# Kernel optimization log

Measured on AMD Instinct MI355X. Metric: run time of the kernel, lower is better.

The kernel has to match this reference:

```python
import jax, jax.numpy as jnp
import numpy as np

N_NODES = 50000
N_EDGES = 800000
D = 64
NEG_SLOPE = 0.01  # torch F.leaky_relu default


def _gin_layer(h, src, dst, eps, W, b, activate):
    # max-aggregate neighbor features: for each dst node, max over incoming src feats
    msg = h[src]  # [E, D] gather
    agg = jax.ops.segment_max(msg, dst, num_segments=N_NODES)  # [N, D]
    # DGL fills nodes with no in-edges with 0 for max reduce
    agg = jnp.where(jnp.isfinite(agg), agg, jnp.zeros((), h.dtype))
    out = ((1.0 + eps) * h + agg) @ W + b
    if activate:
        out = jnp.where(out >= 0, out, NEG_SLOPE * out)
    return out


def setup_inputs() -> dict:
    key = jax.random.key(0)
    ks = jax.random.split(key, 6)
    scale = 1.0 / np.sqrt(D)
    return {
        "n_feat": jax.random.normal(ks[0], (N_NODES, D), dtype=jnp.float32),
        "W0": jax.random.normal(ks[1], (D, D), dtype=jnp.float32) * scale,
        "b0": jnp.zeros((D,), jnp.float32),
        "W1": jax.random.normal(ks[2], (D, D), dtype=jnp.float32) * scale,
        "b1": jnp.zeros((D,), jnp.float32),
        "W2": jax.random.normal(ks[3], (D, D), dtype=jnp.float32) * scale,
        "b2": jnp.zeros((D,), jnp.float32),
        "eps": jnp.zeros((3,), jnp.float32),
        "src": jax.random.randint(ks[4], (N_EDGES,), 0, N_NODES, dtype=jnp.int32),
        "dst": jax.random.randint(ks[5], (N_EDGES,), 0, N_NODES, dtype=jnp.int32),
    }


def reference(n_feat, W0, b0, W1, b1, W2, b2, eps, src, dst):
    h = _gin_layer(n_feat, src, dst, eps[0], W0, b0, activate=True)
    h = _gin_layer(h, src, dst, eps[1], W1, b1, activate=True)
    h = _gin_layer(h, src, dst, eps[2], W2, b2, activate=False)  # last_activate=False
    return h
```

## Files before the change

kernel.cpp:

```cpp
#include <hip/hip_runtime.h>

#define N_NODES 50000
#define N_EDGES 800000
#define D 64
#define CAP 64
#define XLD 72

typedef short short8 __attribute__((ext_vector_type(8)));
typedef float floatx4 __attribute__((ext_vector_type(4)));
typedef unsigned short ushort_t;

__device__ __forceinline__ ushort_t f32_to_bf16(float f) {
    unsigned int u = __float_as_uint(f);
    u += 0x7FFFu + ((u >> 16) & 1u);
    return (ushort_t)(u >> 16);
}
__device__ __forceinline__ float bf16lo(unsigned int u) { return __uint_as_float(u << 16); }
__device__ __forceinline__ float bf16hi(unsigned int u) { return __uint_as_float(u & 0xFFFF0000u); }

__global__ void __launch_bounds__(256) cvtw_kernel(const float* __restrict__ in,
                                                   ushort_t* __restrict__ hb0,
                                                   const float* __restrict__ W0,
                                                   const float* __restrict__ W1,
                                                   const float* __restrict__ W2,
                                                   ushort_t* __restrict__ wt_all) {
    int t = blockIdx.x * 256 + threadIdx.x;
    float4 v = ((const float4*)in)[t];
    uint2 o;
    o.x = ((unsigned)f32_to_bf16(v.y) << 16) | f32_to_bf16(v.x);
    o.y = ((unsigned)f32_to_bf16(v.w) << 16) | f32_to_bf16(v.z);
    ((uint2*)hb0)[t] = o;
    if (blockIdx.x < 3) {
        const float* Ws[3] = {W0, W1, W2};
        const float* W = Ws[blockIdx.x];
        ushort_t* ow = wt_all + blockIdx.x * 4096;
        for (int idx = threadIdx.x; idx < 4096; idx += 256) {
            int k = idx >> 6, n = idx & 63;
            ow[n * 64 + k] = f32_to_bf16(W[idx]);
        }
    }
}

__global__ void __launch_bounds__(256) fill_kernel(const int* __restrict__ src,
                                                   const int* __restrict__ dst,
                                                   int* __restrict__ cnt,
                                                   ushort_t* __restrict__ bucket) {
    int e = blockIdx.x * 256 + threadIdx.x;
    int t = dst[e];
    int slot = atomicAdd(&cnt[t], 1);
    if (slot < CAP) bucket[t * CAP + slot] = (ushort_t)src[e];
}

__global__ void __launch_bounds__(256) layer_kernel(
        const ushort_t* __restrict__ hin,
        const int* __restrict__ cnt,
        const ushort_t* __restrict__ bucket,
        const ushort_t* __restrict__ wt,
        const float* __restrict__ bias,
        const float* __restrict__ eps_arr,
        int layer, int activate, int last,
        ushort_t* __restrict__ out_bf,
        float* __restrict__ out_f32) {
    __shared__ ushort_t bk[16 * CAP];
    __shared__ ushort_t xs[16 * XLD];

    const int tid = threadIdx.x;
    const int lane = tid & 63;
    const int wv = tid >> 6;
    const int grp = lane >> 4;
    const int fo = (lane & 15) * 4;
    const float ev = 1.0f + eps_arr[layer];

    const int r0 = blockIdx.x * 16 + wv * 4;

#pragma unroll
    for (int j = 0; j < 4; ++j)
        bk[(wv * 4 + j) * CAP + lane] = bucket[(r0 + j) * CAP + lane];

    const int rr = r0 + grp;
    int cg = min(cnt[rr], CAP);
    int c0 = __builtin_amdgcn_readlane(cg, 0);
    int c1 = __builtin_amdgcn_readlane(cg, 16);
    int c2 = __builtin_amdgcn_readlane(cg, 32);
    int c3 = __builtin_amdgcn_readlane(cg, 48);
    int cmax = max(max(c0, c1), max(c2, c3));

    const uint2 sv = *(const uint2*)&hin[rr * 64 + fo];

    float m0 = -INFINITY, m1 = -INFINITY, m2 = -INFINITY, m3 = -INFINITY;
    const ushort_t* bkrow = &bk[(wv * 4 + grp) * CAP];
    for (int i = 0; i < cmax; ++i) {
        if (i < cg) {
            int s = bkrow[i];
            const uint2 u = *(const uint2*)&hin[s * 64 + fo];
            m0 = fmaxf(m0, bf16lo(u.x)); m1 = fmaxf(m1, bf16hi(u.x));
            m2 = fmaxf(m2, bf16lo(u.y)); m3 = fmaxf(m3, bf16hi(u.y));
        }
    }
    float a0 = (cg > 0) ? m0 : 0.f, a1 = (cg > 0) ? m1 : 0.f;
    float a2 = (cg > 0) ? m2 : 0.f, a3 = (cg > 0) ? m3 : 0.f;
    float x0 = fmaf(ev, bf16lo(sv.x), a0), x1 = fmaf(ev, bf16hi(sv.x), a1);
    float x2 = fmaf(ev, bf16lo(sv.y), a2), x3 = fmaf(ev, bf16hi(sv.y), a3);
    uint2 w;
    w.x = ((unsigned)f32_to_bf16(x1) << 16) | f32_to_bf16(x0);
    w.y = ((unsigned)f32_to_bf16(x3) << 16) | f32_to_bf16(x2);
    *(uint2*)&xs[(wv * 4 + grp) * XLD + fo] = w;
    __syncthreads();

    const int l15 = lane & 15, hi = lane >> 4;
    const int kc = hi * 8;
    short8 fa0 = *(const short8*)&xs[l15 * XLD + kc];
    short8 fa1 = *(const short8*)&xs[l15 * XLD + 32 + kc];
    const int ncol = wv * 16 + l15;
    short8 fb0 = *(const short8*)&wt[ncol * 64 + kc];
    short8 fb1 = *(const short8*)&wt[ncol * 64 + 32 + kc];
    floatx4 acc = {0.f, 0.f, 0.f, 0.f};
    acc = __builtin_amdgcn_mfma_f32_16x16x32_bf16(fa0, fb0, acc, 0, 0, 0);
    acc = __builtin_amdgcn_mfma_f32_16x16x32_bf16(fa1, fb1, acc, 0, 0, 0);

    const float bv = bias[ncol];
#pragma unroll
    for (int i = 0; i < 4; ++i) {
        int grow = blockIdx.x * 16 + hi * 4 + i;
        float v = acc[i] + bv;
        if (activate) v = (v >= 0.f) ? v : 0.01f * v;
        if (last) out_f32[(size_t)grow * 64 + ncol] = v;
        else out_bf[(size_t)grow * 64 + ncol] = f32_to_bf16(v);
    }
}

extern "C" void kernel_launch(void* const* d_in, const int* in_sizes, int n_in,
                              void* d_out, int out_size, void* d_ws, size_t ws_size,
                              hipStream_t stream) {
    const float* n_feat = (const float*)d_in[0];
    const float* W0 = (const float*)d_in[1];
    const float* b0 = (const float*)d_in[2];
    const float* W1 = (const float*)d_in[3];
    const float* b1 = (const float*)d_in[4];
    const float* W2 = (const float*)d_in[5];
    const float* b2 = (const float*)d_in[6];
    const float* eps = (const float*)d_in[7];
    const int* src = (const int*)d_in[8];
    const int* dst = (const int*)d_in[9];
    float* out = (float*)d_out;

    const size_t BKT_OFF = 200192;
    const size_t HB0_OFF = BKT_OFF + (size_t)N_NODES * CAP * 2;
    const size_t HB1_OFF = HB0_OFF + (size_t)N_NODES * 64 * 2;
    const size_t WT_OFF  = HB1_OFF + (size_t)N_NODES * 64 * 2;

    int* cnt = (int*)d_ws;
    ushort_t* bucket = (ushort_t*)((char*)d_ws + BKT_OFF);
    ushort_t* hb0 = (ushort_t*)((char*)d_ws + HB0_OFF);
    ushort_t* hb1 = (ushort_t*)((char*)d_ws + HB1_OFF);
    ushort_t* wt_all = (ushort_t*)((char*)d_ws + WT_OFF);

    hipMemsetAsync(cnt, 0, (size_t)N_NODES * 4, stream);
    cvtw_kernel<<<3125, 256, 0, stream>>>(n_feat, hb0, W0, W1, W2, wt_all);
    fill_kernel<<<N_EDGES / 256, 256, 0, stream>>>(src, dst, cnt, bucket);

    dim3 blk(256), grd(N_NODES / 16 + 1);

    layer_kernel<<<3125, blk, 0, stream>>>(hb0, cnt, bucket, wt_all,        b0, eps, 0, 1, 0, hb1, out);
    layer_kernel<<<3125, blk, 0, stream>>>(hb1, cnt, bucket, wt_all + 4096, b1, eps, 1, 1, 0, hb0, out);
    layer_kernel<<<3125, blk, 0, stream>>>(hb0, cnt, bucket, wt_all + 8192, b2, eps, 2, 0, 1, hb1, out);
}
```

Before: 212.6 us.

## Unroll neighbor max-gather by four with sentinel padding; fold count zeroing into convert kernel

Neighbor buckets are padded to a multiple of four with a sentinel node index whose feature row holds bf16 -inf. This lets the gather loop load four indices at once and issue four independent row loads per step, raising memory-level parallelism and dropping the per-edge branch. The separate memset of the in-degree counters is replaced by zeroing inside the conversion kernel, which removes one launch. Feature buffers grow by one row for the sentinel, and the loop now reads up to three extra rows per node.

```diff
diff --git a/kernel.cpp b/kernel.cpp
--- a/kernel.cpp
+++ b/kernel.cpp
@@ -5,6 +5,7 @@
 #define D 64
 #define CAP 64
 #define XLD 72
+#define SENT 50000
 
 typedef short short8 __attribute__((ext_vector_type(8)));
 typedef float floatx4 __attribute__((ext_vector_type(4)));
@@ -20,10 +21,12 @@
 
 __global__ void __launch_bounds__(256) cvtw_kernel(const float* __restrict__ in,
                                                    ushort_t* __restrict__ hb0,
+                                                   ushort_t* __restrict__ hb1,
                                                    const float* __restrict__ W0,
                                                    const float* __restrict__ W1,
                                                    const float* __restrict__ W2,
-                                                   ushort_t* __restrict__ wt_all) {
+                                                   ushort_t* __restrict__ wt_all,
+                                                   int* __restrict__ cnt) {
     int t = blockIdx.x * 256 + threadIdx.x;
     float4 v = ((const float4*)in)[t];
     uint2 o;
@@ -38,6 +41,14 @@
             int k = idx >> 6, n = idx & 63;
             ow[n * 64 + k] = f32_to_bf16(W[idx]);
         }
+        if (blockIdx.x == 0) {
+            int l = threadIdx.x;
+            if (l < 64) hb0[(size_t)SENT * 64 + l] = 0xFF80u;
+            else if (l < 128) hb1[(size_t)SENT * 64 + (l - 64)] = 0xFF80u;
+        }
+    } else if (blockIdx.x >= 4 && blockIdx.x < 200) {
+        int i = (blockIdx.x - 4) * 256 + threadIdx.x;
+        if (i < N_NODES) cnt[i] = 0;
     }
 }
 
@@ -68,7 +79,8 @@
     const int lane = tid & 63;
     const int wv = tid >> 6;
     const int grp = lane >> 4;
-    const int fo = (lane & 15) * 4;
+    const int l15 = lane & 15;
+    const int fo = l15 * 4;
     const float ev = 1.0f + eps_arr[layer];
 
     const int r0 = blockIdx.x * 16 + wv * 4;
@@ -78,23 +90,44 @@
         bk[(wv * 4 + j) * CAP + lane] = bucket[(r0 + j) * CAP + lane];
 
     const int rr = r0 + grp;
-    int cg = min(cnt[rr], CAP);
-    int c0 = __builtin_amdgcn_readlane(cg, 0);
-    int c1 = __builtin_amdgcn_readlane(cg, 16);
-    int c2 = __builtin_amdgcn_readlane(cg, 32);
-    int c3 = __builtin_amdgcn_readlane(cg, 48);
-    int cmax = max(max(c0, c1), max(c2, c3));
+    const int cg = min(cnt[rr], CAP);
+    const int c4g = (cg + 3) & ~3;
+    {
+        int s = cg + l15;
+        if (s < c4g) bk[(wv * 4 + grp) * CAP + s] = (ushort_t)SENT;
+    }
+    int c0 = __builtin_amdgcn_readlane(c4g, 0);
+    int c1 = __builtin_amdgcn_readlane(c4g, 16);
+    int c2 = __builtin_amdgcn_readlane(c4g, 32);
+    int c3 = __builtin_amdgcn_readlane(c4g, 48);
+    const int cmax = max(max(c0, c1), max(c2, c3));
 
     const uint2 sv = *(const uint2*)&hin[rr * 64 + fo];
 
     float m0 = -INFINITY, m1 = -INFINITY, m2 = -INFINITY, m3 = -INFINITY;
     const ushort_t* bkrow = &bk[(wv * 4 + grp) * CAP];
-    for (int i = 0; i < cmax; ++i) {
-        if (i < cg) {
-            int s = bkrow[i];
-            const uint2 u = *(const uint2*)&hin[s * 64 + fo];
-            m0 = fmaxf(m0, bf16lo(u.x)); m1 = fmaxf(m1, bf16hi(u.x));
-            m2 = fmaxf(m2, bf16lo(u.y)); m3 = fmaxf(m3, bf16hi(u.y));
+    for (int i = 0; i < cmax; i += 8) {
+        if (i < c4g) {
+            ushort4 s4 = *(const ushort4*)&bkrow[i];
+            uint2 u0 = *(const uint2*)&hin[(int)s4.x * 64 + fo];
+            uint2 u1 = *(const uint2*)&hin[(int)s4.y * 64 + fo];
+            uint2 u2 = *(const uint2*)&hin[(int)s4.z * 64 + fo];
+            uint2 u3 = *(const uint2*)&hin[(int)s4.w * 64 + fo];
+            m0 = fmaxf(m0, fmaxf(fmaxf(bf16lo(u0.x), bf16lo(u1.x)), fmaxf(bf16lo(u2.x), bf16lo(u3.x))));
+            m1 = fmaxf(m1, fmaxf(fmaxf(bf16hi(u0.x), bf16hi(u1.x)), fmaxf(bf16hi(u2.x), bf16hi(u3.x))));
+            m2 = fmaxf(m2, fmaxf(fmaxf(bf16lo(u0.y), bf16lo(u1.y)), fmaxf(bf16lo(u2.y), bf16lo(u3.y))));
+            m3 = fmaxf(m3, fmaxf(fmaxf(bf16hi(u0.y), bf16hi(u1.y)), fmaxf(bf16hi(u2.y), bf16hi(u3.y))));
+        }
+        if (i + 4 < c4g) {
+            ushort4 s4 = *(const ushort4*)&bkrow[i + 4];
+            uint2 u0 = *(const uint2*)&hin[(int)s4.x * 64 + fo];
+            uint2 u1 = *(const uint2*)&hin[(int)s4.y * 64 + fo];
+            uint2 u2 = *(const uint2*)&hin[(int)s4.z * 64 + fo];
+            uint2 u3 = *(const uint2*)&hin[(int)s4.w * 64 + fo];
+            m0 = fmaxf(m0, fmaxf(fmaxf(bf16lo(u0.x), bf16lo(u1.x)), fmaxf(bf16lo(u2.x), bf16lo(u3.x))));
+            m1 = fmaxf(m1, fmaxf(fmaxf(bf16hi(u0.x), bf16hi(u1.x)), fmaxf(bf16hi(u2.x), bf16hi(u3.x))));
+            m2 = fmaxf(m2, fmaxf(fmaxf(bf16lo(u0.y), bf16lo(u1.y)), fmaxf(bf16lo(u2.y), bf16lo(u3.y))));
+            m3 = fmaxf(m3, fmaxf(fmaxf(bf16hi(u0.y), bf16hi(u1.y)), fmaxf(bf16hi(u2.y), bf16hi(u3.y))));
         }
     }
     float a0 = (cg > 0) ? m0 : 0.f, a1 = (cg > 0) ? m1 : 0.f;
@@ -107,7 +140,7 @@
     *(uint2*)&xs[(wv * 4 + grp) * XLD + fo] = w;
     __syncthreads();
 
-    const int l15 = lane & 15, hi = lane >> 4;
+    const int hi = lane >> 4;
     const int kc = hi * 8;
     short8 fa0 = *(const short8*)&xs[l15 * XLD + kc];
     short8 fa1 = *(const short8*)&xs[l15 * XLD + 32 + kc];
@@ -146,8 +179,8 @@
 
     const size_t BKT_OFF = 200192;
     const size_t HB0_OFF = BKT_OFF + (size_t)N_NODES * CAP * 2;
-    const size_t HB1_OFF = HB0_OFF + (size_t)N_NODES * 64 * 2;
-    const size_t WT_OFF  = HB1_OFF + (size_t)N_NODES * 64 * 2;
+    const size_t HB1_OFF = HB0_OFF + (size_t)(N_NODES + 1) * 64 * 2;
+    const size_t WT_OFF  = HB1_OFF + (size_t)(N_NODES + 1) * 64 * 2;
 
     int* cnt = (int*)d_ws;
     ushort_t* bucket = (ushort_t*)((char*)d_ws + BKT_OFF);
@@ -155,11 +188,10 @@
     ushort_t* hb1 = (ushort_t*)((char*)d_ws + HB1_OFF);
     ushort_t* wt_all = (ushort_t*)((char*)d_ws + WT_OFF);
 
-    hipMemsetAsync(cnt, 0, (size_t)N_NODES * 4, stream);
-    cvtw_kernel<<<3125, 256, 0, stream>>>(n_feat, hb0, W0, W1, W2, wt_all);
+    cvtw_kernel<<<3125, 256, 0, stream>>>(n_feat, hb0, hb1, W0, W1, W2, wt_all, cnt);
     fill_kernel<<<N_EDGES / 256, 256, 0, stream>>>(src, dst, cnt, bucket);
 
-    dim3 blk(256), grd(N_NODES / 16 + 1);
+    dim3 blk(256);
 
     layer_kernel<<<3125, blk, 0, stream>>>(hb0, cnt, bucket, wt_all,        b0, eps, 0, 1, 0, hb1, out);
     layer_kernel<<<3125, blk, 0, stream>>>(hb1, cnt, bucket, wt_all + 4096, b1, eps, 1, 1, 0, hb0, out);
```

After: 182.9 us. 1.16x faster.

## Pad neighbor lists with -inf sentinel row and unroll gather by 16; merge prep kernels

Applied to the files above, without the earlier changes.

Neighbor lists in shared memory are padded up to a multiple of 16 with a sentinel node index whose feature row holds bf16 -inf. The gather loop can then issue 16 independent loads per iteration without per-edge bounds checks, which raises memory-level parallelism for the random-access max aggregation. The conversion and bucket-fill kernels are merged into one launch to cut launch overhead. The cost is extra gathers of the sentinel row for short lists and higher register pressure.

```diff
diff --git a/kernel.cpp b/kernel.cpp
--- a/kernel.cpp
+++ b/kernel.cpp
@@ -5,6 +5,7 @@
 #define D 64
 #define CAP 64
 #define XLD 72
+#define SENT 50000
 
 typedef short short8 __attribute__((ext_vector_type(8)));
 typedef float floatx4 __attribute__((ext_vector_type(4)));
@@ -18,38 +19,53 @@
 __device__ __forceinline__ float bf16lo(unsigned int u) { return __uint_as_float(u << 16); }
 __device__ __forceinline__ float bf16hi(unsigned int u) { return __uint_as_float(u & 0xFFFF0000u); }
 
-__global__ void __launch_bounds__(256) cvtw_kernel(const float* __restrict__ in,
-                                                   ushort_t* __restrict__ hb0,
-                                                   const float* __restrict__ W0,
-                                                   const float* __restrict__ W1,
-                                                   const float* __restrict__ W2,
-                                                   ushort_t* __restrict__ wt_all) {
-    int t = blockIdx.x * 256 + threadIdx.x;
-    float4 v = ((const float4*)in)[t];
-    uint2 o;
-    o.x = ((unsigned)f32_to_bf16(v.y) << 16) | f32_to_bf16(v.x);
-    o.y = ((unsigned)f32_to_bf16(v.w) << 16) | f32_to_bf16(v.z);
-    ((uint2*)hb0)[t] = o;
-    if (blockIdx.x < 3) {
-        const float* Ws[3] = {W0, W1, W2};
-        const float* W = Ws[blockIdx.x];
-        ushort_t* ow = wt_all + blockIdx.x * 4096;
-        for (int idx = threadIdx.x; idx < 4096; idx += 256) {
-            int k = idx >> 6, n = idx & 63;
-            ow[n * 64 + k] = f32_to_bf16(W[idx]);
+__global__ void __launch_bounds__(256) prep_kernel(
+        const float* __restrict__ in,
+        ushort_t* __restrict__ hb0,
+        ushort_t* __restrict__ hb1,
+        const float* __restrict__ W0,
+        const float* __restrict__ W1,
+        const float* __restrict__ W2,
+        ushort_t* __restrict__ wt_all,
+        int* __restrict__ cnt,
+        const int* __restrict__ src,
+        const int* __restrict__ dst,
+        ushort_t* __restrict__ bucket) {
+    int b = blockIdx.x;
+    if (b < 3125) {
+        int t = b * 256 + threadIdx.x;
+        float4 v = ((const float4*)in)[t];
+        uint2 o;
+        o.x = ((unsigned)f32_to_bf16(v.y) << 16) | f32_to_bf16(v.x);
+        o.y = ((unsigned)f32_to_bf16(v.w) << 16) | f32_to_bf16(v.z);
+        ((uint2*)hb0)[t] = o;
+        if (b < 3) {
+            const float* Ws[3] = {W0, W1, W2};
+            const float* W = Ws[b];
+            ushort_t* ow = wt_all + b * 4096;
+            for (int idx = threadIdx.x; idx < 4096; idx += 256) {
+                int k = idx >> 6, n = idx & 63;
+                ow[n * 64 + k] = f32_to_bf16(W[idx]);
+            }
+            if (b == 0) {
+                int l = threadIdx.x;
+                if (l < 64) hb0[(size_t)SENT * 64 + l] = 0xFF80u;
+                else if (l < 128) hb1[(size_t)SENT * 64 + (l - 64)] = 0xFF80u;
+            }
         }
+    } else {
+        int e = (b - 3125) * 256 + threadIdx.x;
+        int t = dst[e];
+        int slot = atomicAdd(&cnt[t], 1);
+        if (slot < CAP) bucket[t * CAP + slot] = (ushort_t)src[e];
     }
 }
 
-__global__ void __launch_bounds__(256) fill_kernel(const int* __restrict__ src,
-                                                   const int* __restrict__ dst,
-                                                   int* __restrict__ cnt,
-                                                   ushort_t* __restrict__ bucket) {
-    int e = blockIdx.x * 256 + threadIdx.x;
-    int t = dst[e];
-    int slot = atomicAdd(&cnt[t], 1);
-    if (slot < CAP) bucket[t * CAP + slot] = (ushort_t)src[e];
-}
+#define RED4(ua, ub, uc, ud)                                                                        \
+    m0 = fmaxf(m0, fmaxf(fmaxf(bf16lo(ua.x), bf16lo(ub.x)), fmaxf(bf16lo(uc.x), bf16lo(ud.x))));    \
+    m1 = fmaxf(m1, fmaxf(fmaxf(bf16hi(ua.x), bf16hi(ub.x)), fmaxf(bf16hi(uc.x), bf16hi(ud.x))));    \
+    m2 = fmaxf(m2, fmaxf(fmaxf(bf16lo(ua.y), bf16lo(ub.y)), fmaxf(bf16lo(uc.y), bf16lo(ud.y))));    \
+    m3 = fmaxf(m3, fmaxf(fmaxf(bf16hi(ua.y), bf16hi(ub.y)), fmaxf(bf16hi(uc.y), bf16hi(ud.y))));
 
 __global__ void __launch_bounds__(256) layer_kernel(
         const ushort_t* __restrict__ hin,
@@ -68,7 +84,8 @@
     const int lane = tid & 63;
     const int wv = tid >> 6;
     const int grp = lane >> 4;
-    const int fo = (lane & 15) * 4;
+    const int l15 = lane & 15;
+    const int fo = l15 * 4;
     const float ev = 1.0f + eps_arr[layer];
 
     const int r0 = blockIdx.x * 16 + wv * 4;
@@ -78,24 +95,44 @@
         bk[(wv * 4 + j) * CAP + lane] = bucket[(r0 + j) * CAP + lane];
 
     const int rr = r0 + grp;
-    int cg = min(cnt[rr], CAP);
-    int c0 = __builtin_amdgcn_readlane(cg, 0);
-    int c1 = __builtin_amdgcn_readlane(cg, 16);
-    int c2 = __builtin_amdgcn_readlane(cg, 32);
-    int c3 = __builtin_amdgcn_readlane(cg, 48);
-    int cmax = max(max(c0, c1), max(c2, c3));
+    const int cg = min(cnt[rr], CAP);
+    int g0 = __builtin_amdgcn_readlane(cg, 0);
+    int g1 = __builtin_amdgcn_readlane(cg, 16);
+    int g2 = __builtin_amdgcn_readlane(cg, 32);
+    int g3 = __builtin_amdgcn_readlane(cg, 48);
+    const int cmax = (max(max(g0, g1), max(g2, g3)) + 15) & ~15;
+
+    ushort_t* bkrow = &bk[(wv * 4 + grp) * CAP];
+    for (int s = cg + l15; s < cmax; s += 16) bkrow[s] = (ushort_t)SENT;
 
     const uint2 sv = *(const uint2*)&hin[rr * 64 + fo];
 
     float m0 = -INFINITY, m1 = -INFINITY, m2 = -INFINITY, m3 = -INFINITY;
-    const ushort_t* bkrow = &bk[(wv * 4 + grp) * CAP];
-    for (int i = 0; i < cmax; ++i) {
-        if (i < cg) {
-            int s = bkrow[i];
-            const uint2 u = *(const uint2*)&hin[s * 64 + fo];
-            m0 = fmaxf(m0, bf16lo(u.x)); m1 = fmaxf(m1, bf16hi(u.x));
-            m2 = fmaxf(m2, bf16lo(u.y)); m3 = fmaxf(m3, bf16hi(u.y));
-        }
+    for (int i = 0; i < cmax; i += 16) {
+        ushort4 sa = *(const ushort4*)&bkrow[i];
+        ushort4 sb = *(const ushort4*)&bkrow[i + 4];
+        ushort4 sc = *(const ushort4*)&bkrow[i + 8];
+        ushort4 sd = *(const ushort4*)&bkrow[i + 12];
+        uint2 u0  = *(const uint2*)&hin[(int)sa.x * 64 + fo];
+        uint2 u1  = *(const uint2*)&hin[(int)sa.y * 64 + fo];
+        uint2 u2  = *(const uint2*)&hin[(int)sa.z * 64 + fo];
+        uint2 u3  = *(const uint2*)&hin[(int)sa.w * 64 + fo];
+        uint2 u4  = *(const uint2*)&hin[(int)sb.x * 64 + fo];
+        uint2 u5  = *(const uint2*)&hin[(int)sb.y * 64 + fo];
+        uint2 u6  = *(const uint2*)&hin[(int)sb.z * 64 + fo];
+        uint2 u7  = *(const uint2*)&hin[(int)sb.w * 64 + fo];
+        uint2 u8  = *(const uint2*)&hin[(int)sc.x * 64 + fo];
+        uint2 u9  = *(const uint2*)&hin[(int)sc.y * 64 + fo];
+        uint2 u10 = *(const uint2*)&hin[(int)sc.z * 64 + fo];
+        uint2 u11 = *(const uint2*)&hin[(int)sc.w * 64 + fo];
+        uint2 u12 = *(const uint2*)&hin[(int)sd.x * 64 + fo];
+        uint2 u13 = *(const uint2*)&hin[(int)sd.y * 64 + fo];
+        uint2 u14 = *(const uint2*)&hin[(int)sd.z * 64 + fo];
+        uint2 u15 = *(const uint2*)&hin[(int)sd.w * 64 + fo];
+        RED4(u0, u1, u2, u3)
+        RED4(u4, u5, u6, u7)
+        RED4(u8, u9, u10, u11)
+        RED4(u12, u13, u14, u15)
     }
     float a0 = (cg > 0) ? m0 : 0.f, a1 = (cg > 0) ? m1 : 0.f;
     float a2 = (cg > 0) ? m2 : 0.f, a3 = (cg > 0) ? m3 : 0.f;
@@ -107,7 +144,7 @@
     *(uint2*)&xs[(wv * 4 + grp) * XLD + fo] = w;
     __syncthreads();
 
-    const int l15 = lane & 15, hi = lane >> 4;
+    const int hi = lane >> 4;
     const int kc = hi * 8;
     short8 fa0 = *(const short8*)&xs[l15 * XLD + kc];
     short8 fa1 = *(const short8*)&xs[l15 * XLD + 32 + kc];
@@ -146,8 +183,8 @@
 
     const size_t BKT_OFF = 200192;
     const size_t HB0_OFF = BKT_OFF + (size_t)N_NODES * CAP * 2;
-    const size_t HB1_OFF = HB0_OFF + (size_t)N_NODES * 64 * 2;
-    const size_t WT_OFF  = HB1_OFF + (size_t)N_NODES * 64 * 2;
+    const size_t HB1_OFF = HB0_OFF + (size_t)(N_NODES + 1) * 64 * 2;
+    const size_t WT_OFF  = HB1_OFF + (size_t)(N_NODES + 1) * 64 * 2;
 
     int* cnt = (int*)d_ws;
     ushort_t* bucket = (ushort_t*)((char*)d_ws + BKT_OFF);
@@ -156,11 +193,10 @@
     ushort_t* wt_all = (ushort_t*)((char*)d_ws + WT_OFF);
 
     hipMemsetAsync(cnt, 0, (size_t)N_NODES * 4, stream);
-    cvtw_kernel<<<3125, 256, 0, stream>>>(n_feat, hb0, W0, W1, W2, wt_all);
-    fill_kernel<<<N_EDGES / 256, 256, 0, stream>>>(src, dst, cnt, bucket);
-
-    dim3 blk(256), grd(N_NODES / 16 + 1);
-
+    prep_kernel<<<6250, 256, 0, stream>>>(n_feat, hb0, hb1, W0, W1, W2, wt_all,
+                                          cnt, src, dst, bucket);
+
+    dim3 blk(256);
     layer_kernel<<<3125, blk, 0, stream>>>(hb0, cnt, bucket, wt_all,        b0, eps, 0, 1, 0, hb1, out);
     layer_kernel<<<3125, blk, 0, stream>>>(hb1, cnt, bucket, wt_all + 4096, b1, eps, 1, 1, 0, hb0, out);
     layer_kernel<<<3125, blk, 0, stream>>>(hb0, cnt, bucket, wt_all + 8192, b2, eps, 2, 0, 1, hb1, out);
```

Result: faster. 202.8 us (-4.6%).
